# Optimization experiments

Measured on AMD Instinct MI355X. Metric: run time of the kernel, lower is better.

Reference implementation:

```python
import jax, jax.numpy as jnp
import numpy as np

TEMPERATURE = 0.5
LAMBDA_REG = 0.1
NUM_GROUPS = 4  # number of distinct sensitive-attribute values
EPS = 1e-8      # torch cosine_similarity norm clamp


def setup_inputs() -> dict:
    key = jax.random.key(0)
    k1, k2, k3 = jax.random.split(key, 3)
    B, D = 4096, 256
    return {
        "z_i": jax.random.normal(k1, (B, D), dtype=jnp.float32),
        "z_j": jax.random.normal(k2, (B, D), dtype=jnp.float32),
        "sensitive_features": jax.random.randint(k3, (B,), 0, NUM_GROUPS, dtype=jnp.int64),
    }


def reference(z_i, z_j, sensitive_features):
    B = z_i.shape[0]
    z = jnp.concatenate([z_i, z_j], axis=0)                       # [2B, D]
    norm = jnp.maximum(jnp.linalg.norm(z, axis=1, keepdims=True), EPS)
    zn = z / norm                                                  # row-normalized
    S = zn @ zn.T                                                  # [2B, 2B] cosine sims

    # NT-Xent contrastive term
    pos = jnp.concatenate([jnp.diagonal(S, offset=B), jnp.diagonal(S, offset=-B)])  # [2B]
    mask = 1.0 - jnp.eye(2 * B, dtype=S.dtype)                     # zero out self-sims
    den = jnp.sum(mask * jnp.exp(S / TEMPERATURE), axis=1)         # [2B]
    contrastive = jnp.sum(-(pos / TEMPERATURE) + jnp.log(den)) / (2 * B)

    # Fairness penalty over groups of the FIRST B rows (indices come from sensitive_features)
    Sg = S[:B, :B]
    onehot = jax.nn.one_hot(sensitive_features, NUM_GROUPS, dtype=S.dtype)  # [B, G]
    group_sums = jnp.sum(onehot * (Sg @ onehot), axis=0)           # [G] sum_{i,j in g} S[i,j] (incl. diag, as torch)
    counts = jnp.sum(onehot, axis=0)                               # [G]
    per_group = jnp.where(counts > 1, group_sums / (counts * (counts - 1.0)), 0.0)
    num_unique = jnp.sum(counts > 0).astype(S.dtype)
    fairness = LAMBDA_REG * (jnp.sum(per_group) / num_unique)

    return contrastive + fairness
```

## Files before the change

### kernel.cpp

```cpp
#include <hip/hip_runtime.h>
#include <hip/hip_bf16.h>

typedef __attribute__((ext_vector_type(8))) short short8;
typedef __attribute__((ext_vector_type(4))) float f32x4;
typedef __attribute__((address_space(1))) const void gvoid_t;
typedef __attribute__((address_space(3))) void lvoid_t;

#define NB 4096
#define DD 256
#define TWOB 8192
#define NMACRO 1056u
#define GSUM_BLOCKS 16

__device__ __forceinline__ unsigned short f2bf(float f) {
  unsigned int u = __float_as_uint(f);
  u += 0x7fffu + ((u >> 16) & 1u);
  return (unsigned short)(u >> 16);
}
__device__ __forceinline__ float bf2f(unsigned short s) {
  return __uint_as_float(((unsigned int)s) << 16);
}


__global__ __launch_bounds__(256) void norm_kernel(const float* __restrict__ zi,
                                                   const float* __restrict__ zj,
                                                   float* __restrict__ wsf,
                                                   float* __restrict__ ppos,
                                                   unsigned short* __restrict__ znb) {
  __shared__ float sred[4];
  if (blockIdx.x < 32) wsf[blockIdx.x * 256 + threadIdx.x] = 0.f;
  const int lane = threadIdx.x & 63, wave = threadIdx.x >> 6;
  const int i = blockIdx.x * 4 + wave;

  float4 a = ((const float4*)(zi + (size_t)i * DD))[lane];
  float4 b = ((const float4*)(zj + (size_t)i * DD))[lane];
  float sa = a.x * a.x + a.y * a.y + a.z * a.z + a.w * a.w;
  float sb = b.x * b.x + b.y * b.y + b.z * b.z + b.w * b.w;
  float sab = a.x * b.x + a.y * b.y + a.z * b.z + a.w * b.w;
#pragma unroll
  for (int m = 32; m >= 1; m >>= 1) {
    sa += __shfl_xor(sa, m);
    sb += __shfl_xor(sb, m);
    sab += __shfl_xor(sab, m);
  }
  float ra = 1.0f / fmaxf(sqrtf(sa), 1e-8f);
  float rb = 1.0f / fmaxf(sqrtf(sb), 1e-8f);
  ushort4 oa, ob;
  oa.x = f2bf(a.x * ra); oa.y = f2bf(a.y * ra); oa.z = f2bf(a.z * ra); oa.w = f2bf(a.w * ra);
  ob.x = f2bf(b.x * rb); ob.y = f2bf(b.y * rb); ob.z = f2bf(b.z * rb); ob.w = f2bf(b.w * rb);
  ((ushort4*)(znb + (size_t)i * DD))[lane] = oa;
  ((ushort4*)(znb + (size_t)(i + NB) * DD))[lane] = ob;

  if (lane == 0) sred[wave] = sab * ra * rb;
  __syncthreads();
  if (threadIdx.x == 0)
    ppos[blockIdx.x] = sred[0] + sred[1] + sred[2] + sred[3];
}

__global__ __launch_bounds__(256, 2) void den_kernel(const int* __restrict__ sf,
                                                     float* __restrict__ wsf,
                                                     const unsigned short* __restrict__ znb,
                                                     float* __restrict__ vsum_part,
                                                     int* __restrict__ cnt_part) {
  __shared__ __align__(16) unsigned short As[2][4096];
  __shared__ __align__(16) unsigned short Bs[2][8192];

  float* den = wsf;

  const int tid = threadIdx.x;
  const int lane = tid & 63, wave = tid >> 6;
  const unsigned t_lin = blockIdx.y * 64u + blockIdx.x;

  if (t_lin < GSUM_BLOCKS) {
    const int b = (int)t_lin;
    const int r0 = b * 256;
    float acc[4][4];
#pragma unroll
    for (int q = 0; q < 4; ++q)
#pragma unroll
      for (int e = 0; e < 4; ++e) acc[q][e] = 0.f;
    int cnt[4] = {0, 0, 0, 0};
    const int rw = r0 + wave * 64;
    for (int k = 0; k < 64; ++k) {
      int row = rw + k;
      int g = sf[row];
      ushort4 v = ((const ushort4*)(znb + (size_t)row * DD))[lane];
      float f0 = bf2f(v.x), f1 = bf2f(v.y), f2 = bf2f(v.z), f3 = bf2f(v.w);
#pragma unroll
      for (int q = 0; q < 4; ++q) {
        bool sel = (g == q);
        acc[q][0] += sel ? f0 : 0.f;
        acc[q][1] += sel ? f1 : 0.f;
        acc[q][2] += sel ? f2 : 0.f;
        acc[q][3] += sel ? f3 : 0.f;
        cnt[q] += sel ? 1 : 0;
      }
    }
    float4* lsd = (float4*)&As[0][0];
    int* lcnt = (int*)&Bs[0][0];
#pragma unroll
    for (int q = 0; q < 4; ++q) {
      float4 t;
      t.x = acc[q][0]; t.y = acc[q][1]; t.z = acc[q][2]; t.w = acc[q][3];
      lsd[(wave * 4 + q) * 64 + lane] = t;
    }
    if (lane == 0) {
#pragma unroll
      for (int q = 0; q < 4; ++q) lcnt[wave * 4 + q] = cnt[q];
    }
    __syncthreads();
    {
      int g = tid >> 6, l = tid & 63;
      float4 s0 = lsd[(0 + g) * 64 + l];
      float4 s1 = lsd[(4 + g) * 64 + l];
      float4 s2 = lsd[(8 + g) * 64 + l];
      float4 s3 = lsd[(12 + g) * 64 + l];
      float4 s;
      s.x = s0.x + s1.x + s2.x + s3.x;
      s.y = s0.y + s1.y + s2.y + s3.y;
      s.z = s0.z + s1.z + s2.z + s3.z;
      s.w = s0.w + s1.w + s2.w + s3.w;
      ((float4*)(vsum_part + (size_t)(b * 4 + g) * 256))[l] = s;
      if (tid < 4)
        cnt_part[b * 4 + tid] = lcnt[tid] + lcnt[4 + tid] + lcnt[8 + tid] + lcnt[12 + tid];
    }
    return;
  }
  if (t_lin >= NMACRO + GSUM_BLOCKS) return;

  unsigned t = t_lin - GSUM_BLOCKS;
  unsigned tr = 0;
  while (t >= 32u - (tr >> 1)) { t -= 32u - (tr >> 1); ++tr; }
  unsigned c = (tr >> 1) + t;
  const size_t rowbase = (size_t)tr * 128;
  const size_t colbase = (size_t)c * 256;
  const int tc0 = (int)(2 * c), tc1 = (int)(2 * c + 1);

  const int u = lane >> 3;
  const int cp = (lane & 7) ^ u;
  const int ri = 2 * u + (cp >> 2);
  const int kelem = (cp & 3) * 8;
  const int slot = ((((lane & 1) << 2) | (lane >> 4)) ^ ((lane >> 1) & 7));
  const int fragoff = ((lane & 15) >> 1) * 128 + slot * 16;
  const int wrow = wave & 1, wcol = wave >> 1;

  const int tch = wcol ? tc1 : tc0;
  const float fr = (tch >= (int)tr) ? 1.f : 0.f;
  const float fc = (tch > (int)tr) ? 1.f : 0.f;

  f32x4 zero = {0.f, 0.f, 0.f, 0.f};
  f32x4 acc[4][8];
#pragma unroll
  for (int i = 0; i < 4; ++i)
#pragma unroll
    for (int j = 0; j < 8; ++j) acc[i][j] = zero;

  auto stage = [&](int kt, int buf) {
#pragma unroll
    for (int j = 0; j < 2; ++j) {
      int is = wave * 2 + j;
      const unsigned short* gpa = znb + (rowbase + is * 16 + ri) * DD + kt * 32 + kelem;
      __builtin_amdgcn_global_load_lds((gvoid_t*)gpa, (lvoid_t*)&As[buf][is * 512], 16, 0, 0);
    }
#pragma unroll
    for (int j = 0; j < 4; ++j) {
      int is = wave * 4 + j;
      const unsigned short* gpb = znb + (colbase + is * 16 + ri) * DD + kt * 32 + kelem;
      __builtin_amdgcn_global_load_lds((gvoid_t*)gpb, (lvoid_t*)&Bs[buf][is * 512], 16, 0, 0);
    }
  };

  stage(0, 0);
  __syncthreads();
#pragma unroll
  for (int kt = 0; kt < 8; ++kt) {
    if (kt < 7) stage(kt + 1, (kt + 1) & 1);
    const int buf = kt & 1;
    short8 af[4], bfr[8];
#pragma unroll
    for (int mi = 0; mi < 4; ++mi)
      af[mi] = *(const short8*)((const char*)&As[0][0] + buf * 8192 + wrow * 4096 + mi * 1024 + fragoff);
#pragma unroll
    for (int ni = 0; ni < 8; ++ni)
      bfr[ni] = *(const short8*)((const char*)&Bs[0][0] + buf * 16384 + wcol * 8192 + ni * 1024 + fragoff);
#pragma unroll
    for (int mi = 0; mi < 4; ++mi)
#pragma unroll
      for (int ni = 0; ni < 8; ++ni)
        acc[mi][ni] = __builtin_amdgcn_mfma_f32_16x16x32_bf16(af[mi], bfr[ni], acc[mi][ni], 0, 0, 0);
    __syncthreads();
  }

  float rsum[4][4];
  float csum[8];
#pragma unroll
  for (int mi = 0; mi < 4; ++mi)
#pragma unroll
    for (int r = 0; r < 4; ++r) rsum[mi][r] = 0.f;
#pragma unroll
  for (int ni = 0; ni < 8; ++ni) csum[ni] = 0.f;
#pragma unroll
  for (int mi = 0; mi < 4; ++mi)
#pragma unroll
    for (int ni = 0; ni < 8; ++ni)
#pragma unroll
      for (int r = 0; r < 4; ++r) {
        float e = __expf(2.0f * acc[mi][ni][r]);
        rsum[mi][r] += e;
        csum[ni] += e;
      }
#pragma unroll
  for (int m = 1; m < 16; m <<= 1)
#pragma unroll
    for (int mi = 0; mi < 4; ++mi)
#pragma unroll
      for (int r = 0; r < 4; ++r) rsum[mi][r] += __shfl_xor(rsum[mi][r], m);
#pragma unroll
  for (int m = 16; m < 64; m <<= 1)
#pragma unroll
    for (int ni = 0; ni < 8; ++ni) csum[ni] += __shfl_xor(csum[ni], m);

  float* Lr = (float*)&As[0][0];
  float* Lc = Lr + 256;
  if ((lane & 15) == 0) {
    int h = lane >> 4;
#pragma unroll
    for (int mi = 0; mi < 4; ++mi)
#pragma unroll
      for (int r = 0; r < 4; ++r)
        Lr[wcol * 128 + wrow * 64 + mi * 16 + h * 4 + r] = rsum[mi][r] * fr;
  }
  if (lane < 16) {
#pragma unroll
    for (int ni = 0; ni < 8; ++ni)
      Lc[wrow * 256 + wcol * 128 + ni * 16 + lane] = csum[ni] * fc;
  }
  __syncthreads();
  if (tid < 128) {
    unsafeAtomicAdd(&den[rowbase + tid], Lr[tid] + Lr[128 + tid]);
  }
  {
    float v = Lc[tid] + Lc[256 + tid];
    if (v != 0.f) unsafeAtomicAdd(&den[colbase + tid], v);
  }
}

__global__ __launch_bounds__(256) void tail_kernel(const float* __restrict__ wsf,
                                                   const float* __restrict__ vsum_part,
                                                   const int* __restrict__ cnt_part,
                                                   const float* __restrict__ ppos,
                                                   float* __restrict__ out) {
  __shared__ float sred[32];
  const float* den = wsf;
  const int tid = threadIdx.x;
  const int lane = tid & 63, wave = tid >> 6;

  const float e2 = __expf(2.0f);
  float ls = 0.f;
  for (int i = tid; i < TWOB; i += 256) ls += __logf(den[i] - e2);
#pragma unroll
  for (int m = 32; m >= 1; m >>= 1) ls += __shfl_xor(ls, m);
  if (lane == 0) sred[wave] = ls;

  float pp = 0.f;
#pragma unroll
  for (int k = 0; k < 4; ++k) pp += ppos[k * 256 + tid];
#pragma unroll
  for (int m = 32; m >= 1; m >>= 1) pp += __shfl_xor(pp, m);
  if (lane == 0) sred[4 + wave] = pp;

  float gp[4];
#pragma unroll
  for (int g = 0; g < 4; ++g) {
    float v = 0.f;
#pragma unroll
    for (int b = 0; b < 16; ++b) v += vsum_part[(size_t)(b * 4 + g) * 256 + tid];
    gp[g] = v * v;
#pragma unroll
    for (int m = 32; m >= 1; m >>= 1) gp[g] += __shfl_xor(gp[g], m);
  }
  if (lane == 0) {
#pragma unroll
    for (int g = 0; g < 4; ++g) sred[8 + wave * 4 + g] = gp[g];
  }
  __syncthreads();
  if (tid == 0) {
    float lsum = sred[0] + sred[1] + sred[2] + sred[3];
    float psum = sred[4] + sred[5] + sred[6] + sred[7];
    float contrastive = (lsum - 4.0f * psum) / (float)TWOB;
    float fsum = 0.f;
    int uniq = 0;
#pragma unroll
    for (int q = 0; q < 4; ++q) {
      int ci = 0;
#pragma unroll
      for (int b = 0; b < 16; ++b) ci += cnt_part[b * 4 + q];
      float gsq = sred[8 + q] + sred[12 + q] + sred[16 + q] + sred[20 + q];
      float c = (float)ci;
      if (ci > 0) uniq++;
      if (ci > 1) fsum += gsq / (c * (c - 1.0f));
    }
    out[0] = contrastive + 0.1f * (fsum / (uniq > 0 ? (float)uniq : 1.0f));
  }
}

extern "C" void kernel_launch(void* const* d_in, const int* in_sizes, int n_in,
                              void* d_out, int out_size, void* d_ws, size_t ws_size,
                              hipStream_t stream) {
  const float* zi = (const float*)d_in[0];
  const float* zj = (const float*)d_in[1];
  const int* sf = (const int*)d_in[2];
  float* out = (float*)d_out;
  char* ws = (char*)d_ws;
  float* wsf = (float*)ws;
  unsigned short* znb = (unsigned short*)(ws + 65536);
  float* vsum_part = (float*)(ws + 4259840);
  int* cnt_part = (int*)(ws + 4276224);
  float* ppos = (float*)(ws + 4276480);

  hipLaunchKernelGGL(norm_kernel, dim3(1024), dim3(256), 0, stream, zi, zj, wsf, ppos, znb);
  hipLaunchKernelGGL(den_kernel, dim3(64, 17), dim3(256), 0, stream,
                     sf, wsf, znb, vsum_part, cnt_part);
  hipLaunchKernelGGL(tail_kernel, dim3(1), dim3(256), 0, stream,
                     wsf, vsum_part, cnt_part, ppos, out);
}
```

Before: 108.3 us.

## Triple-buffer GEMM loads and fuse tail reduction via last-block counter

The den kernel's LDS staging moves from double to triple buffering. It uses explicit vmcnt waits and a single barrier per k-step, and raises wave priority around the MFMA block, so loads for step k+2 overlap compute. The separate single-block tail kernel is removed: each block increments a global done counter, and the last block performs the final log/positive/fairness reduction. This saves one kernel launch. The cost is more LDS per block (which may reduce occupancy) and an atomic counter plus fences on every block.

```diff
diff --git a/kernel.cpp b/kernel.cpp
--- a/kernel.cpp
+++ b/kernel.cpp
@@ -11,6 +11,7 @@
 #define TWOB 8192
 #define NMACRO 1056u
 #define GSUM_BLOCKS 16
+#define NPART 1072
 
 __device__ __forceinline__ unsigned short f2bf(float f) {
   unsigned int u = __float_as_uint(f);
@@ -29,6 +30,7 @@
                                                    unsigned short* __restrict__ znb) {
   __shared__ float sred[4];
   if (blockIdx.x < 32) wsf[blockIdx.x * 256 + threadIdx.x] = 0.f;
+  if (blockIdx.x == 32 && threadIdx.x == 0) ((int*)(wsf + 8192))[0] = 0;
   const int lane = threadIdx.x & 63, wave = threadIdx.x >> 6;
   const int i = blockIdx.x * 4 + wave;
 
@@ -61,15 +63,21 @@
                                                      float* __restrict__ wsf,
                                                      const unsigned short* __restrict__ znb,
                                                      float* __restrict__ vsum_part,
-                                                     int* __restrict__ cnt_part) {
-  __shared__ __align__(16) unsigned short As[2][4096];
-  __shared__ __align__(16) unsigned short Bs[2][8192];
+                                                     int* __restrict__ cnt_part,
+                                                     const float* __restrict__ ppos,
+                                                     float* __restrict__ out,
+                                                     int* __restrict__ done_cnt) {
+  __shared__ __align__(16) unsigned short As[3][4096];
+  __shared__ __align__(16) unsigned short Bs[3][8192];
+  __shared__ int islast;
 
   float* den = wsf;
 
   const int tid = threadIdx.x;
   const int lane = tid & 63, wave = tid >> 6;
   const unsigned t_lin = blockIdx.y * 64u + blockIdx.x;
+
+  if (t_lin >= NMACRO + GSUM_BLOCKS) return;
 
   if (t_lin < GSUM_BLOCKS) {
     const int b = (int)t_lin;
@@ -124,183 +132,197 @@
       if (tid < 4)
         cnt_part[b * 4 + tid] = lcnt[tid] + lcnt[4 + tid] + lcnt[8 + tid] + lcnt[12 + tid];
     }
-    return;
+  } else {
+    unsigned t = t_lin - GSUM_BLOCKS;
+    unsigned tr = 0;
+    while (t >= 32u - (tr >> 1)) { t -= 32u - (tr >> 1); ++tr; }
+    unsigned c = (tr >> 1) + t;
+    const size_t rowbase = (size_t)tr * 128;
+    const size_t colbase = (size_t)c * 256;
+    const int tc0 = (int)(2 * c), tc1 = (int)(2 * c + 1);
+
+    const int u = lane >> 3;
+    const int cp = (lane & 7) ^ u;
+    const int ri = 2 * u + (cp >> 2);
+    const int kelem = (cp & 3) * 8;
+    const int slot = ((((lane & 1) << 2) | (lane >> 4)) ^ ((lane >> 1) & 7));
+    const int fragoff = ((lane & 15) >> 1) * 128 + slot * 16;
+    const int wrow = wave & 1, wcol = wave >> 1;
+
+    const int tch = wcol ? tc1 : tc0;
+    const float fr = (tch >= (int)tr) ? 1.f : 0.f;
+    const float fc = (tch > (int)tr) ? 1.f : 0.f;
+
+    f32x4 zero = {0.f, 0.f, 0.f, 0.f};
+    f32x4 acc[4][8];
+#pragma unroll
+    for (int i = 0; i < 4; ++i)
+#pragma unroll
+      for (int j = 0; j < 8; ++j) acc[i][j] = zero;
+
+    auto stage = [&](int kt, int buf) {
+#pragma unroll
+      for (int j = 0; j < 2; ++j) {
+        int is = wave * 2 + j;
+        const unsigned short* gpa = znb + (rowbase + is * 16 + ri) * DD + kt * 32 + kelem;
+        __builtin_amdgcn_global_load_lds((gvoid_t*)gpa, (lvoid_t*)&As[buf][is * 512], 16, 0, 0);
+      }
+#pragma unroll
+      for (int j = 0; j < 4; ++j) {
+        int is = wave * 4 + j;
+        const unsigned short* gpb = znb + (colbase + is * 16 + ri) * DD + kt * 32 + kelem;
+        __builtin_amdgcn_global_load_lds((gvoid_t*)gpb, (lvoid_t*)&Bs[buf][is * 512], 16, 0, 0);
+      }
+    };
+
+    stage(0, 0);
+    stage(1, 1);
+#pragma unroll
+    for (int kt = 0; kt < 8; ++kt) {
+      const int buf = kt % 3;
+      if (kt < 7) asm volatile("s_waitcnt vmcnt(6)" ::: "memory");
+      else        asm volatile("s_waitcnt vmcnt(0)" ::: "memory");
+      __builtin_amdgcn_s_barrier();
+      asm volatile("" ::: "memory");
+      short8 af[4], bfr[8];
+#pragma unroll
+      for (int mi = 0; mi < 4; ++mi)
+        af[mi] = *(const short8*)((const char*)&As[0][0] + buf * 8192 + wrow * 4096 + mi * 1024 + fragoff);
+#pragma unroll
+      for (int ni = 0; ni < 8; ++ni)
+        bfr[ni] = *(const short8*)((const char*)&Bs[0][0] + buf * 16384 + wcol * 8192 + ni * 1024 + fragoff);
+      if (kt < 6) stage(kt + 2, (kt + 2) % 3);
+      __builtin_amdgcn_s_setprio(1);
+#pragma unroll
+      for (int mi = 0; mi < 4; ++mi)
+#pragma unroll
+        for (int ni = 0; ni < 8; ++ni)
+          acc[mi][ni] = __builtin_amdgcn_mfma_f32_16x16x32_bf16(af[mi], bfr[ni], acc[mi][ni], 0, 0, 0);
+      __builtin_amdgcn_s_setprio(0);
+      asm volatile("" ::: "memory");
+    }
+
+    float rsum[4][4];
+    float csum[8];
+#pragma unroll
+    for (int mi = 0; mi < 4; ++mi)
+#pragma unroll
+      for (int r = 0; r < 4; ++r) rsum[mi][r] = 0.f;
+#pragma unroll
+    for (int ni = 0; ni < 8; ++ni) csum[ni] = 0.f;
+#pragma unroll
+    for (int mi = 0; mi < 4; ++mi)
+#pragma unroll
+      for (int ni = 0; ni < 8; ++ni)
+#pragma unroll
+        for (int r = 0; r < 4; ++r) {
+          float e = __expf(2.0f * acc[mi][ni][r]);
+          rsum[mi][r] += e;
+          csum[ni] += e;
+        }
+#pragma unroll
+    for (int m = 1; m < 16; m <<= 1)
+#pragma unroll
+      for (int mi = 0; mi < 4; ++mi)
+#pragma unroll
+        for (int r = 0; r < 4; ++r) rsum[mi][r] += __shfl_xor(rsum[mi][r], m);
+#pragma unroll
+    for (int m = 16; m < 64; m <<= 1)
+#pragma unroll
+      for (int ni = 0; ni < 8; ++ni) csum[ni] += __shfl_xor(csum[ni], m);
+
+    float* Lr = (float*)&As[0][0];
+    float* Lc = Lr + 256;
+    if ((lane & 15) == 0) {
+      int h = lane >> 4;
+#pragma unroll
+      for (int mi = 0; mi < 4; ++mi)
+#pragma unroll
+        for (int r = 0; r < 4; ++r)
+          Lr[wcol * 128 + wrow * 64 + mi * 16 + h * 4 + r] = rsum[mi][r] * fr;
+    }
+    if (lane < 16) {
+#pragma unroll
+      for (int ni = 0; ni < 8; ++ni)
+        Lc[wrow * 256 + wcol * 128 + ni * 16 + lane] = csum[ni] * fc;
+    }
+    __syncthreads();
+    if (tid < 128) {
+      unsafeAtomicAdd(&den[rowbase + tid], Lr[tid] + Lr[128 + tid]);
+    }
+    {
+      float v = Lc[tid] + Lc[256 + tid];
+      if (v != 0.f) unsafeAtomicAdd(&den[colbase + tid], v);
+    }
   }
-  if (t_lin >= NMACRO + GSUM_BLOCKS) return;
-
-  unsigned t = t_lin - GSUM_BLOCKS;
-  unsigned tr = 0;
-  while (t >= 32u - (tr >> 1)) { t -= 32u - (tr >> 1); ++tr; }
-  unsigned c = (tr >> 1) + t;
-  const size_t rowbase = (size_t)tr * 128;
-  const size_t colbase = (size_t)c * 256;
-  const int tc0 = (int)(2 * c), tc1 = (int)(2 * c + 1);
-
-  const int u = lane >> 3;
-  const int cp = (lane & 7) ^ u;
-  const int ri = 2 * u + (cp >> 2);
-  const int kelem = (cp & 3) * 8;
-  const int slot = ((((lane & 1) << 2) | (lane >> 4)) ^ ((lane >> 1) & 7));
-  const int fragoff = ((lane & 15) >> 1) * 128 + slot * 16;
-  const int wrow = wave & 1, wcol = wave >> 1;
-
-  const int tch = wcol ? tc1 : tc0;
-  const float fr = (tch >= (int)tr) ? 1.f : 0.f;
-  const float fc = (tch > (int)tr) ? 1.f : 0.f;
-
-  f32x4 zero = {0.f, 0.f, 0.f, 0.f};
-  f32x4 acc[4][8];
-#pragma unroll
-  for (int i = 0; i < 4; ++i)
-#pragma unroll
-    for (int j = 0; j < 8; ++j) acc[i][j] = zero;
-
-  auto stage = [&](int kt, int buf) {
-#pragma unroll
-    for (int j = 0; j < 2; ++j) {
-      int is = wave * 2 + j;
-      const unsigned short* gpa = znb + (rowbase + is * 16 + ri) * DD + kt * 32 + kelem;
-      __builtin_amdgcn_global_load_lds((gvoid_t*)gpa, (lvoid_t*)&As[buf][is * 512], 16, 0, 0);
-    }
-#pragma unroll
-    for (int j = 0; j < 4; ++j) {
-      int is = wave * 4 + j;
-      const unsigned short* gpb = znb + (colbase + is * 16 + ri) * DD + kt * 32 + kelem;
-      __builtin_amdgcn_global_load_lds((gvoid_t*)gpb, (lvoid_t*)&Bs[buf][is * 512], 16, 0, 0);
-    }
-  };
-
-  stage(0, 0);
+
   __syncthreads();
-#pragma unroll
-  for (int kt = 0; kt < 8; ++kt) {
-    if (kt < 7) stage(kt + 1, (kt + 1) & 1);
-    const int buf = kt & 1;
-    short8 af[4], bfr[8];
-#pragma unroll
-    for (int mi = 0; mi < 4; ++mi)
-      af[mi] = *(const short8*)((const char*)&As[0][0] + buf * 8192 + wrow * 4096 + mi * 1024 + fragoff);
-#pragma unroll
-    for (int ni = 0; ni < 8; ++ni)
-      bfr[ni] = *(const short8*)((const char*)&Bs[0][0] + buf * 16384 + wcol * 8192 + ni * 1024 + fragoff);
-#pragma unroll
-    for (int mi = 0; mi < 4; ++mi)
-#pragma unroll
-      for (int ni = 0; ni < 8; ++ni)
-        acc[mi][ni] = __builtin_amdgcn_mfma_f32_16x16x32_bf16(af[mi], bfr[ni], acc[mi][ni], 0, 0, 0);
-    __syncthreads();
-  }
-
-  float rsum[4][4];
-  float csum[8];
-#pragma unroll
-  for (int mi = 0; mi < 4; ++mi)
-#pragma unroll
-    for (int r = 0; r < 4; ++r) rsum[mi][r] = 0.f;
-#pragma unroll
-  for (int ni = 0; ni < 8; ++ni) csum[ni] = 0.f;
-#pragma unroll
-  for (int mi = 0; mi < 4; ++mi)
-#pragma unroll
-    for (int ni = 0; ni < 8; ++ni)
-#pragma unroll
-      for (int r = 0; r < 4; ++r) {
-        float e = __expf(2.0f * acc[mi][ni][r]);
-        rsum[mi][r] += e;
-        csum[ni] += e;
-      }
-#pragma unroll
-  for (int m = 1; m < 16; m <<= 1)
-#pragma unroll
-    for (int mi = 0; mi < 4; ++mi)
-#pragma unroll
-      for (int r = 0; r < 4; ++r) rsum[mi][r] += __shfl_xor(rsum[mi][r], m);
-#pragma unroll
-  for (int m = 16; m < 64; m <<= 1)
-#pragma unroll
-    for (int ni = 0; ni < 8; ++ni) csum[ni] += __shfl_xor(csum[ni], m);
-
-  float* Lr = (float*)&As[0][0];
-  float* Lc = Lr + 256;
-  if ((lane & 15) == 0) {
-    int h = lane >> 4;
-#pragma unroll
-    for (int mi = 0; mi < 4; ++mi)
-#pragma unroll
-      for (int r = 0; r < 4; ++r)
-        Lr[wcol * 128 + wrow * 64 + mi * 16 + h * 4 + r] = rsum[mi][r] * fr;
-  }
-  if (lane < 16) {
-#pragma unroll
-    for (int ni = 0; ni < 8; ++ni)
-      Lc[wrow * 256 + wcol * 128 + ni * 16 + lane] = csum[ni] * fc;
+  if (tid == 0) {
+    __threadfence();
+    int prev = atomicAdd(done_cnt, 1);
+    islast = (prev == NPART - 1) ? 1 : 0;
   }
   __syncthreads();
-  if (tid < 128) {
-    unsafeAtomicAdd(&den[rowbase + tid], Lr[tid] + Lr[128 + tid]);
-  }
+  if (islast == 0) return;
+  if (tid == 0) __threadfence();
+  __syncthreads();
+
   {
-    float v = Lc[tid] + Lc[256 + tid];
-    if (v != 0.f) unsafeAtomicAdd(&den[colbase + tid], v);
-  }
-}
-
-__global__ __launch_bounds__(256) void tail_kernel(const float* __restrict__ wsf,
-                                                   const float* __restrict__ vsum_part,
-                                                   const int* __restrict__ cnt_part,
-                                                   const float* __restrict__ ppos,
-                                                   float* __restrict__ out) {
-  __shared__ float sred[32];
-  const float* den = wsf;
-  const int tid = threadIdx.x;
-  const int lane = tid & 63, wave = tid >> 6;
-
-  const float e2 = __expf(2.0f);
-  float ls = 0.f;
-  for (int i = tid; i < TWOB; i += 256) ls += __logf(den[i] - e2);
-#pragma unroll
-  for (int m = 32; m >= 1; m >>= 1) ls += __shfl_xor(ls, m);
-  if (lane == 0) sred[wave] = ls;
-
-  float pp = 0.f;
-#pragma unroll
-  for (int k = 0; k < 4; ++k) pp += ppos[k * 256 + tid];
-#pragma unroll
-  for (int m = 32; m >= 1; m >>= 1) pp += __shfl_xor(pp, m);
-  if (lane == 0) sred[4 + wave] = pp;
-
-  float gp[4];
-#pragma unroll
-  for (int g = 0; g < 4; ++g) {
-    float v = 0.f;
-#pragma unroll
-    for (int b = 0; b < 16; ++b) v += vsum_part[(size_t)(b * 4 + g) * 256 + tid];
-    gp[g] = v * v;
-#pragma unroll
-    for (int m = 32; m >= 1; m >>= 1) gp[g] += __shfl_xor(gp[g], m);
-  }
-  if (lane == 0) {
-#pragma unroll
-    for (int g = 0; g < 4; ++g) sred[8 + wave * 4 + g] = gp[g];
-  }
-  __syncthreads();
-  if (tid == 0) {
-    float lsum = sred[0] + sred[1] + sred[2] + sred[3];
-    float psum = sred[4] + sred[5] + sred[6] + sred[7];
-    float contrastive = (lsum - 4.0f * psum) / (float)TWOB;
-    float fsum = 0.f;
-    int uniq = 0;
-#pragma unroll
-    for (int q = 0; q < 4; ++q) {
-      int ci = 0;
-#pragma unroll
-      for (int b = 0; b < 16; ++b) ci += cnt_part[b * 4 + q];
-      float gsq = sred[8 + q] + sred[12 + q] + sred[16 + q] + sred[20 + q];
-      float c = (float)ci;
-      if (ci > 0) uniq++;
-      if (ci > 1) fsum += gsq / (c * (c - 1.0f));
-    }
-    out[0] = contrastive + 0.1f * (fsum / (uniq > 0 ? (float)uniq : 1.0f));
+    float* sred = (float*)&Bs[0][0];
+    const float e2 = __expf(2.0f);
+    float ls = 0.f;
+    for (int i = tid; i < TWOB; i += 256) {
+      float d = __hip_atomic_load(&wsf[i], __ATOMIC_RELAXED, __HIP_MEMORY_SCOPE_AGENT);
+      ls += __logf(d - e2);
+    }
+#pragma unroll
+    for (int m = 32; m >= 1; m >>= 1) ls += __shfl_xor(ls, m);
+    if (lane == 0) sred[wave] = ls;
+
+    float pp = 0.f;
+#pragma unroll
+    for (int k = 0; k < 4; ++k) pp += ppos[k * 256 + tid];
+#pragma unroll
+    for (int m = 32; m >= 1; m >>= 1) pp += __shfl_xor(pp, m);
+    if (lane == 0) sred[4 + wave] = pp;
+
+    float gp[4];
+#pragma unroll
+    for (int g = 0; g < 4; ++g) {
+      float v = 0.f;
+#pragma unroll
+      for (int b = 0; b < 16; ++b)
+        v += __hip_atomic_load(&vsum_part[(size_t)(b * 4 + g) * 256 + tid],
+                               __ATOMIC_RELAXED, __HIP_MEMORY_SCOPE_AGENT);
+      gp[g] = v * v;
+#pragma unroll
+      for (int m = 32; m >= 1; m >>= 1) gp[g] += __shfl_xor(gp[g], m);
+    }
+    if (lane == 0) {
+#pragma unroll
+      for (int g = 0; g < 4; ++g) sred[8 + wave * 4 + g] = gp[g];
+    }
+    __syncthreads();
+    if (tid == 0) {
+      float lsum = sred[0] + sred[1] + sred[2] + sred[3];
+      float psum = sred[4] + sred[5] + sred[6] + sred[7];
+      float contrastive = (lsum - 4.0f * psum) / (float)TWOB;
+      float fsum = 0.f;
+      int uniq = 0;
+#pragma unroll
+      for (int q = 0; q < 4; ++q) {
+        int ci = 0;
+#pragma unroll
+        for (int b = 0; b < 16; ++b)
+          ci += __hip_atomic_load(&cnt_part[b * 4 + q],
+                                  __ATOMIC_RELAXED, __HIP_MEMORY_SCOPE_AGENT);
+        float gsq = sred[8 + q] + sred[12 + q] + sred[16 + q] + sred[20 + q];
+        float cf = (float)ci;
+        if (ci > 0) uniq++;
+        if (ci > 1) fsum += gsq / (cf * (cf - 1.0f));
+      }
+      out[0] = contrastive + 0.1f * (fsum / (uniq > 0 ? (float)uniq : 1.0f));
+    }
   }
 }
 
@@ -313,6 +335,7 @@
   float* out = (float*)d_out;
   char* ws = (char*)d_ws;
   float* wsf = (float*)ws;
+  int* done_cnt = (int*)(ws + 32768);
   unsigned short* znb = (unsigned short*)(ws + 65536);
   float* vsum_part = (float*)(ws + 4259840);
   int* cnt_part = (int*)(ws + 4276224);
@@ -320,7 +343,5 @@
 
   hipLaunchKernelGGL(norm_kernel, dim3(1024), dim3(256), 0, stream, zi, zj, wsf, ppos, znb);
   hipLaunchKernelGGL(den_kernel, dim3(64, 17), dim3(256), 0, stream,
-                     sf, wsf, znb, vsum_part, cnt_part);
-  hipLaunchKernelGGL(tail_kernel, dim3(1), dim3(256), 0, stream,
-                     wsf, vsum_part, cnt_part, ppos, out);
-}
+                     sf, wsf, znb, vsum_part, cnt_part, ppos, out, done_cnt);
+}
```

Result: slower. 120.2 us (+11.0%).

## Replace atomic den accumulation with partial buffers and parallel reduction kernel

Applied to the files above, without the earlier changes.

The similarity kernel now writes its per-tile row and column exp-sums to dedicated partial buffers instead of issuing float atomics into a shared den array. A new 64-block reduction kernel sums those partials, applies the log, and hands per-block results to the tail kernel, which no longer loops over all 8192 rows on a single block. This removes atomic contention, the zero-init step, and the serial single-block log loop. In exchange it adds an extra kernel launch and several MB of partial-buffer writes and reads.

```diff
diff --git a/kernel.cpp b/kernel.cpp
--- a/kernel.cpp
+++ b/kernel.cpp
@@ -24,11 +24,9 @@
 
 __global__ __launch_bounds__(256) void norm_kernel(const float* __restrict__ zi,
                                                    const float* __restrict__ zj,
-                                                   float* __restrict__ wsf,
                                                    float* __restrict__ ppos,
                                                    unsigned short* __restrict__ znb) {
   __shared__ float sred[4];
-  if (blockIdx.x < 32) wsf[blockIdx.x * 256 + threadIdx.x] = 0.f;
   const int lane = threadIdx.x & 63, wave = threadIdx.x >> 6;
   const int i = blockIdx.x * 4 + wave;
 
@@ -58,14 +56,13 @@
 }
 
 __global__ __launch_bounds__(256, 2) void den_kernel(const int* __restrict__ sf,
-                                                     float* __restrict__ wsf,
                                                      const unsigned short* __restrict__ znb,
                                                      float* __restrict__ vsum_part,
-                                                     int* __restrict__ cnt_part) {
+                                                     int* __restrict__ cnt_part,
+                                                     float* __restrict__ rowpart,
+                                                     float* __restrict__ colpart) {
   __shared__ __align__(16) unsigned short As[2][4096];
   __shared__ __align__(16) unsigned short Bs[2][8192];
-
-  float* den = wsf;
 
   const int tid = threadIdx.x;
   const int lane = tid & 63, wave = tid >> 6;
@@ -237,27 +234,47 @@
   }
   __syncthreads();
   if (tid < 128) {
-    unsafeAtomicAdd(&den[rowbase + tid], Lr[tid] + Lr[128 + tid]);
-  }
-  {
-    float v = Lc[tid] + Lc[256 + tid];
-    if (v != 0.f) unsafeAtomicAdd(&den[colbase + tid], v);
-  }
-}
-
-__global__ __launch_bounds__(256) void tail_kernel(const float* __restrict__ wsf,
+    rowpart[(size_t)(tr * 32u + (c - (tr >> 1))) * 128 + tid] = Lr[tid] + Lr[128 + tid];
+  }
+  colpart[((size_t)c * 64 + tr) * 256 + tid] = Lc[tid] + Lc[256 + tid];
+}
+
+__global__ __launch_bounds__(128) void denred_kernel(const float* __restrict__ rowpart,
+                                                     const float* __restrict__ colpart,
+                                                     float* __restrict__ lsred) {
+  __shared__ float sred2[2];
+  const int b = blockIdx.x;
+  const int tid = threadIdx.x;
+  const int lane = tid & 63, wave = tid >> 6;
+
+  float s = 0.f;
+  const int jmax = 32 - (b >> 1);
+  const float* rp = rowpart + (size_t)b * 32 * 128 + tid;
+  for (int j = 0; j < jmax; ++j) s += rp[j * 128];
+
+  const int cc = b >> 1;
+  const int trmax = (2 * cc + 1 < 63) ? (2 * cc + 1) : 63;
+  const float* cpp = colpart + ((size_t)cc * 64) * 256 + (b & 1) * 128 + tid;
+  for (int t2 = 0; t2 <= trmax; ++t2) s += cpp[(size_t)t2 * 256];
+
+  float ls = __logf(s - __expf(2.0f));
+#pragma unroll
+  for (int m = 32; m >= 1; m >>= 1) ls += __shfl_xor(ls, m);
+  if (lane == 0) sred2[wave] = ls;
+  __syncthreads();
+  if (tid == 0) lsred[b] = sred2[0] + sred2[1];
+}
+
+__global__ __launch_bounds__(256) void tail_kernel(const float* __restrict__ lsred,
                                                    const float* __restrict__ vsum_part,
                                                    const int* __restrict__ cnt_part,
                                                    const float* __restrict__ ppos,
                                                    float* __restrict__ out) {
   __shared__ float sred[32];
-  const float* den = wsf;
   const int tid = threadIdx.x;
   const int lane = tid & 63, wave = tid >> 6;
 
-  const float e2 = __expf(2.0f);
-  float ls = 0.f;
-  for (int i = tid; i < TWOB; i += 256) ls += __logf(den[i] - e2);
+  float ls = (tid < 64) ? lsred[tid] : 0.f;
 #pragma unroll
   for (int m = 32; m >= 1; m >>= 1) ls += __shfl_xor(ls, m);
   if (lane == 0) sred[wave] = ls;
@@ -296,9 +313,9 @@
 #pragma unroll
       for (int b = 0; b < 16; ++b) ci += cnt_part[b * 4 + q];
       float gsq = sred[8 + q] + sred[12 + q] + sred[16 + q] + sred[20 + q];
-      float c = (float)ci;
+      float cf = (float)ci;
       if (ci > 0) uniq++;
-      if (ci > 1) fsum += gsq / (c * (c - 1.0f));
+      if (ci > 1) fsum += gsq / (cf * (cf - 1.0f));
     }
     out[0] = contrastive + 0.1f * (fsum / (uniq > 0 ? (float)uniq : 1.0f));
   }
@@ -312,15 +329,18 @@
   const int* sf = (const int*)d_in[2];
   float* out = (float*)d_out;
   char* ws = (char*)d_ws;
-  float* wsf = (float*)ws;
+  float* lsred = (float*)ws;
+  float* ppos = (float*)(ws + 1024);
+  int* cnt_part = (int*)(ws + 8192);
+  float* vsum_part = (float*)(ws + 16384);
   unsigned short* znb = (unsigned short*)(ws + 65536);
-  float* vsum_part = (float*)(ws + 4259840);
-  int* cnt_part = (int*)(ws + 4276224);
-  float* ppos = (float*)(ws + 4276480);
-
-  hipLaunchKernelGGL(norm_kernel, dim3(1024), dim3(256), 0, stream, zi, zj, wsf, ppos, znb);
+  float* rowpart = (float*)(ws + 4259840);
+  float* colpart = (float*)(ws + 5308416);
+
+  hipLaunchKernelGGL(norm_kernel, dim3(1024), dim3(256), 0, stream, zi, zj, ppos, znb);
   hipLaunchKernelGGL(den_kernel, dim3(64, 17), dim3(256), 0, stream,
-                     sf, wsf, znb, vsum_part, cnt_part);
+                     sf, znb, vsum_part, cnt_part, rowpart, colpart);
+  hipLaunchKernelGGL(denred_kernel, dim3(64), dim3(128), 0, stream, rowpart, colpart, lsred);
   hipLaunchKernelGGL(tail_kernel, dim3(1), dim3(256), 0, stream,
-                     wsf, vsum_part, cnt_part, ppos, out);
-}
+                     lsred, vsum_part, cnt_part, ppos, out);
+}
```

After: 116.8 us. +7.8%, slower.
